# Kernel tuning notes

Hardware: AMD Instinct MI355X
Metric: run time of the kernel (lower is better)

The kernel has to match this reference:

```python
import jax, jax.numpy as jnp
import numpy as np

N, E = 100000, 800000
IN, HID, H, C, L, OUT = 32, 128, 4, 32, 3, 5
NEG_SLOPE = 0.2
EPS = 1e-5


def setup_inputs() -> dict:
    key = jax.random.key(0)
    ks = jax.random.split(key, 20)
    s = 0.1
    inp = {
        "x": jax.random.normal(ks[0], (N, IN), jnp.float32),
        "edge_index": jax.random.randint(ks[1], (2, E), 0, N, jnp.int64),
        "edge_attr": jax.random.uniform(ks[2], (E, 1), jnp.float32),
        "Win": jax.random.normal(ks[3], (IN, HID), jnp.float32) * s,
        "b_in": jnp.zeros((HID,), jnp.float32),
        "Wg": jax.random.normal(ks[4], (L, HID, H * C), jnp.float32) * s,
        "bg": jnp.zeros((L, H * C), jnp.float32),
        "a_src": jax.random.normal(ks[5], (L, H, C), jnp.float32) * s,
        "a_dst": jax.random.normal(ks[6], (L, H, C), jnp.float32) * s,
        "We": jax.random.normal(ks[7], (L, 1, H * C), jnp.float32) * s,
        "a_edge": jax.random.normal(ks[8], (L, H, C), jnp.float32) * s,
        "ln_w": jnp.ones((L, HID), jnp.float32),
        "ln_b": jnp.zeros((L, HID), jnp.float32),
        "Wout": jax.random.normal(ks[9], (HID, OUT), jnp.float32) * s,
        "bout": jnp.zeros((OUT,), jnp.float32),
    }
    return inp


def _add_self_loops(src, dst, ea):
    # PyG fill_value='mean': self-loop attr = mean of incoming edge attrs per node
    ones = jnp.ones((src.shape[0],), ea.dtype)
    deg = jax.ops.segment_sum(ones, dst, N)
    loop_attr = jax.ops.segment_sum(ea, dst, N) / jnp.maximum(deg, 1.0)[:, None]
    idx = jnp.arange(N, dtype=src.dtype)
    return (jnp.concatenate([src, idx]), jnp.concatenate([dst, idx]),
            jnp.concatenate([ea, loop_attr], axis=0))


def _gat_conv(x, src, dst, ea, Wg, bg, a_s, a_d, We, a_e):
    xh = (x @ Wg).reshape(N, H, C)                    # [N,H,C]
    al_s = jnp.einsum('nhc,hc->nh', xh, a_s)          # [N,H]
    al_d = jnp.einsum('nhc,hc->nh', xh, a_d)
    ee = (ea @ We).reshape(-1, H, C)                  # [Et,H,C]
    al_e = jnp.einsum('ehc,hc->eh', ee, a_e)
    logits = jax.nn.leaky_relu(al_s[src] + al_d[dst] + al_e, NEG_SLOPE)
    m = jax.ops.segment_max(logits, dst, N)
    m = jnp.where(jnp.isfinite(m), m, 0.0)
    ex = jnp.exp(logits - m[dst])
    den = jax.ops.segment_sum(ex, dst, N)
    alpha = ex / (den[dst] + 1e-16)                   # segment softmax over dst
    out = jax.ops.segment_sum(alpha[:, :, None] * xh[src], dst, N)
    return out.reshape(N, H * C) + bg


def _graph_layernorm(h, w, b):
    # PyG LayerNorm(mode='graph'): normalize over all nodes and features
    h = h - jnp.mean(h)
    var = jnp.mean(h * h)
    return h / jnp.sqrt(var + EPS) * w + b


def reference(x, edge_index, edge_attr, Win, b_in, Wg, bg, a_src, a_dst, We,
              a_edge, ln_w, ln_b, Wout, bout):
    src, dst = edge_index[0], edge_index[1]
    src, dst, ea = _add_self_loops(src, dst, edge_attr)
    h = x @ Win + b_in
    for l in range(L):
        g = _gat_conv(h, src, dst, ea, Wg[l], bg[l], a_src[l], a_dst[l],
                      We[l], a_edge[l])
        g = _graph_layernorm(g, ln_w[l], ln_b[l])
        h = jax.nn.relu(g + h)
    return h @ Wout + bout
```

## Files before the change

kernel.cpp:

```cpp
#include <hip/hip_runtime.h>
#include <hip/hip_bf16.h>

#define NN 100000
#define EE 800000
#define HID 128
#define NH 4
#define CH 32
#define NL 3
#define NOUT 5
#define NEG_SLOPE 0.2f
#define LN_EPS 1e-5f
#define GCAP 64
#define NB_SCAN 98
#define HQ (HID / 2)
#define WB_LSZ 9216
#define HB 3125
#define NG64 1563

typedef unsigned int u32;
typedef __attribute__((ext_vector_type(8))) short bf16x8;
typedef __attribute__((ext_vector_type(4))) float f32x4;

static __device__ __forceinline__ float bflo(u32 r) { return __uint_as_float(r << 16); }
static __device__ __forceinline__ float bfhi(u32 r) { return __uint_as_float(r & 0xffff0000u); }
static __device__ __forceinline__ unsigned short f2bf(float x) {
    union U { __hip_bfloat16 b; unsigned short s; } u;
    u.b = __float2bfloat16(x);
    return u.s;
}
static __device__ __forceinline__ u32 pack2(float a, float b) {
    return (u32)f2bf(a) | ((u32)f2bf(b) << 16);
}
static __device__ __forceinline__ float lrelu(float x) {
    return x > 0.f ? x : NEG_SLOPE * x;
}

__global__ void hist_prep_kernel(const int* __restrict__ ei, int* __restrict__ cnt,
                                 u32* __restrict__ slot,
                                 const float* __restrict__ We, const float* __restrict__ a_e,
                                 float* __restrict__ wedot,
                                 const float* __restrict__ Win, const float* __restrict__ b_in,
                                 const float* __restrict__ Wg, float* __restrict__ wf,
                                 const float* __restrict__ a_src, const float* __restrict__ a_dst,
                                 u32* __restrict__ wb, float* __restrict__ wga) {
    int b = blockIdx.x, t = threadIdx.x;
    if (b < HB) {
        int e = b * 256 + t;
        if (e >= EE) return;
        int d = ei[EE + e];
        int s = atomicAdd(&cnt[d], 1);
        slot[e] = ((u32)d << 8) | (u32)s;
        return;
    }
    if (b == HB) {
        if (t < NL * NH) {
            int l = t >> 2, hh = t & 3;
            float s = 0.f;
            #pragma unroll
            for (int c = 0; c < CH; c++)
                s += We[l * HID + hh * CH + c] * a_e[l * HID + hh * CH + c];
            wedot[t] = s;
        }
        for (int i = t; i < HID * 8; i += 256) {
            int m = i >> 3, j = i & 7;
            int hh = j & 3;
            const float* a = (j < 4) ? (a_src + hh * CH) : (a_dst + hh * CH);
            const float* wrow = Wg + (size_t)m * HID + hh * CH;
            float s = 0.f;
            #pragma unroll
            for (int c = 0; c < CH; c++) s += wrow[c] * a[c];
            wga[i] = s;
        }
        return;
    }
    if (b < HB + 18) {
        int idx = (b - HB - 1) * 256 + t;
        if (idx >= 33 * HID) return;
        int r = idx >> 7, c = idx & 127;
        float acc = 0.f;
        for (int k = 0; k < HID; k++) {
            float a = (r < 32) ? Win[r * HID + k] : b_in[k];
            acc += a * Wg[(size_t)k * HID + c];
        }
        wf[r * HID + c] = acc;
        return;
    }
    {
        int idx = (b - HB - 18) * 256 + t;
        if (idx >= 2 * 2304) return;
        int l = idx / 2304;
        int rem = idx % 2304;
        int ks = rem / 576;
        int ct = (rem % 576) / 64;
        int lane = rem % 64;
        int q = lane >> 4, n = lane & 15;
        const float* W = Wg + (size_t)(l + 1) * HID * HID;
        float v[8];
        if (ct < 8) {
            #pragma unroll
            for (int j = 0; j < 8; j++) {
                int k = ks * 32 + q * 8 + j;
                v[j] = W[(size_t)k * HID + ct * 16 + n];
            }
        } else {
            #pragma unroll
            for (int j = 0; j < 8; j++) v[j] = 0.f;
            if (n < 8) {
                const float* a = (n < 4) ? (a_src + (l + 1) * HID + (n & 3) * CH)
                                         : (a_dst + (l + 1) * HID + (n & 3) * CH);
                #pragma unroll
                for (int j = 0; j < 8; j++) {
                    int k = ks * 32 + q * 8 + j;
                    const float* wrow = W + (size_t)k * HID + (n & 3) * CH;
                    float s = 0.f;
                    for (int c = 0; c < CH; c++) s += wrow[c] * a[c];
                    v[j] = s;
                }
            }
        }
        u32* dst = wb + (size_t)l * WB_LSZ + (size_t)((ks * 9 + ct) * 64 + lane) * 4;
        dst[0] = pack2(v[0], v[1]); dst[1] = pack2(v[2], v[3]);
        dst[2] = pack2(v[4], v[5]); dst[3] = pack2(v[6], v[7]);
    }
}

__global__ __launch_bounds__(1024) void scan1_kernel(const int* __restrict__ cnt,
                                                     int* __restrict__ rowptr,
                                                     int* __restrict__ bsum) {
    __shared__ int ws[16];
    int gid = blockIdx.x * 1024 + threadIdx.x;
    int v = (gid < NN) ? cnt[gid] : 0;
    int lane = threadIdx.x & 63, wid = threadIdx.x >> 6;
    int s = v;
    #pragma unroll
    for (int off = 1; off < 64; off <<= 1) {
        int t = __shfl_up(s, off, 64);
        if (lane >= off) s += t;
    }
    if (lane == 63) ws[wid] = s;
    __syncthreads();
    int add = 0;
    for (int w2 = 0; w2 < wid; w2++) add += ws[w2];
    int incl = s + add;
    if (gid <= NN) rowptr[gid] = incl - v;
    if (threadIdx.x == 1023) bsum[blockIdx.x] = incl;
}

__global__ void scan2_prep2_kernel(int* __restrict__ bsum,
                                   const float* __restrict__ Win,
                                   const float* __restrict__ b_in,
                                   const float* __restrict__ wga,
                                   float* __restrict__ wf, u32* __restrict__ wb2) {
    if (blockIdx.x == 0) {
        __shared__ int w0tot_s;
        int tid = threadIdx.x;
        int v = (tid < NB_SCAN) ? bsum[tid] : 0;
        int lane = tid & 63, wid = tid >> 6;
        int s = v;
        #pragma unroll
        for (int off = 1; off < 64; off <<= 1) {
            int t = __shfl_up(s, off, 64);
            if (lane >= off) s += t;
        }
        if (wid == 0 && lane == 63) w0tot_s = s;
        __syncthreads();
        int incl = s + (wid ? w0tot_s : 0);
        if (tid < NB_SCAN) bsum[tid] = incl - v;
        return;
    }
    int b = blockIdx.x - 1;
    int lane = threadIdx.x;
    if (lane >= 64) return;
    int q = lane >> 4, n = lane & 15;
    if (b == 17) {
        if (lane < 8) {
            float s = 0.f;
            for (int m = 0; m < HID; m++) s += b_in[m] * wga[m * 8 + lane];
            wf[33 * HID + lane] = s;
        }
        return;
    }
    float v[8];
    if (b < 8) {
        #pragma unroll
        for (int j = 0; j < 8; j++) v[j] = Win[(q * 8 + j) * HID + b * 16 + n];
    } else if (b < 16) {
        int ct = b - 8;
        #pragma unroll
        for (int j = 0; j < 8; j++) v[j] = wf[(q * 8 + j) * HID + ct * 16 + n];
    } else {
        #pragma unroll
        for (int j = 0; j < 8; j++) v[j] = 0.f;
        if (n < 8) {
            #pragma unroll
            for (int j = 0; j < 8; j++) {
                const float* wrow = Win + (q * 8 + j) * HID;
                float s = 0.f;
                for (int m = 0; m < HID; m++) s += wrow[m] * wga[m * 8 + n];
                v[j] = s;
            }
        }
    }
    u32* dst = wb2 + (size_t)(b * 64 + lane) * 4;
    dst[0] = pack2(v[0], v[1]); dst[1] = pack2(v[2], v[3]);
    dst[2] = pack2(v[4], v[5]); dst[3] = pack2(v[6], v[7]);
}

__global__ void scan3_kernel(int* __restrict__ rowptr, const int* __restrict__ bsum) {
    int gid = blockIdx.x * 1024 + threadIdx.x;
    if (gid <= NN) rowptr[gid] += bsum[blockIdx.x];
}

__global__ __launch_bounds__(256) void scatter_ingemm_kernel(
        const int* __restrict__ ei, const float* __restrict__ ea,
        const int* __restrict__ rowptr, const u32* __restrict__ slot,
        uint2* __restrict__ edges,
        const float* __restrict__ x, const u32* __restrict__ wb2,
        const float* __restrict__ wf, const float* __restrict__ b_in,
        u32* __restrict__ h, u32* __restrict__ xh,
        float* __restrict__ al_s, float* __restrict__ al_d) {
    __shared__ u32 xsu[1024];
    if (blockIdx.x < HB) {
        int e = blockIdx.x * 256 + threadIdx.x;
        if (e >= EE) return;
        u32 p = slot[e];
        int d = (int)(p >> 8);
        int pos = rowptr[d] + (int)(p & 255u);
        edges[pos] = make_uint2((u32)ei[e], __float_as_uint(ea[e]));
        return;
    }
    int t = threadIdx.x;
    int wv = t >> 6, lane = t & 63;
    int q = lane >> 4, n16 = lane & 15;
    int n0 = (blockIdx.x - HB) * 64;
    {
        int row = t >> 2, qq = t & 3;
        int gr = n0 + row;
        int rt = row >> 4, m = row & 15;
        uint4 op = make_uint4(0u, 0u, 0u, 0u);
        if (gr < NN) {
            float4 vA = *(const float4*)&x[(size_t)gr * 32 + qq * 8];
            float4 vB = *(const float4*)&x[(size_t)gr * 32 + qq * 8 + 4];
            op.x = pack2(vA.x, vA.y); op.y = pack2(vA.z, vA.w);
            op.z = pack2(vB.x, vB.y); op.w = pack2(vB.z, vB.w);
        }
        *(uint4*)&xsu[(rt * 64 + qq * 16 + m) * 4] = op;
    }
    bf16x8 bwin[2], bwf[2], bal;
    #pragma unroll
    for (int cc = 0; cc < 2; cc++) {
        uint4 r0 = *(const uint4*)&wb2[(size_t)(((wv * 2 + cc)) * 64 + lane) * 4];
        uint4 r1 = *(const uint4*)&wb2[(size_t)((8 + wv * 2 + cc) * 64 + lane) * 4];
        bwin[cc] = __builtin_bit_cast(bf16x8, r0);
        bwf[cc]  = __builtin_bit_cast(bf16x8, r1);
    }
    {
        uint4 r = *(const uint4*)&wb2[(size_t)(16 * 64 + lane) * 4];
        bal = __builtin_bit_cast(bf16x8, r);
    }
    __syncthreads();
    f32x4 acch[4][2], accx[4][2], accal[4];
    #pragma unroll
    for (int rt = 0; rt < 4; rt++) {
        acch[rt][0] = (f32x4){0.f, 0.f, 0.f, 0.f};
        acch[rt][1] = (f32x4){0.f, 0.f, 0.f, 0.f};
        accx[rt][0] = (f32x4){0.f, 0.f, 0.f, 0.f};
        accx[rt][1] = (f32x4){0.f, 0.f, 0.f, 0.f};
        accal[rt]   = (f32x4){0.f, 0.f, 0.f, 0.f};
    }
    #pragma unroll
    for (int rt = 0; rt < 4; rt++) {
        uint4 araw = *(const uint4*)&xsu[(rt * 64 + lane) * 4];
        bf16x8 af = __builtin_bit_cast(bf16x8, araw);
        acch[rt][0] = __builtin_amdgcn_mfma_f32_16x16x32_bf16(af, bwin[0], acch[rt][0], 0, 0, 0);
        acch[rt][1] = __builtin_amdgcn_mfma_f32_16x16x32_bf16(af, bwin[1], acch[rt][1], 0, 0, 0);
        accx[rt][0] = __builtin_amdgcn_mfma_f32_16x16x32_bf16(af, bwf[0], accx[rt][0], 0, 0, 0);
        accx[rt][1] = __builtin_amdgcn_mfma_f32_16x16x32_bf16(af, bwf[1], accx[rt][1], 0, 0, 0);
        if (wv == 3)
            accal[rt] = __builtin_amdgcn_mfma_f32_16x16x32_bf16(af, bal, accal[rt], 0, 0, 0);
    }
    float bi[2], bfv[2];
    #pragma unroll
    for (int cc = 0; cc < 2; cc++) {
        int col = (wv * 2 + cc) * 16 + n16;
        bi[cc] = b_in[col];
        bfv[cc] = wf[32 * HID + col];
    }
    float bfa = (wv == 3 && n16 < 8) ? wf[33 * HID + n16] : 0.f;
    #pragma unroll
    for (int rt = 0; rt < 4; rt++) {
        #pragma unroll
        for (int reg = 0; reg < 4; reg++) {
            int row = n0 + rt * 16 + q * 4 + reg;
            #pragma unroll
            for (int cc = 0; cc < 2; cc++) {
                float v = acch[rt][cc][reg] + bi[cc];
                float vp = __shfl_xor(v, 1, 64);
                float u = accx[rt][cc][reg] + bfv[cc];
                float up = __shfl_xor(u, 1, 64);
                if (!(n16 & 1) && row < NN) {
                    int colp = (wv * 2 + cc) * 8 + (n16 >> 1);
                    h[(size_t)row * HQ + colp] = pack2(v, vp);
                    xh[(size_t)row * HQ + colp] = pack2(u, up);
                }
            }
            if (wv == 3 && row < NN && n16 < 8) {
                float v = accal[rt][reg] + bfa;
                if (n16 < 4) al_s[row * 4 + n16] = v;
                else         al_d[row * 4 + (n16 - 4)] = v;
            }
        }
    }
}

__global__ __launch_bounds__(256) void gemm_mfma_kernel(const u32* __restrict__ h,
        const u32* __restrict__ wb, u32* __restrict__ xh, const u32* __restrict__ g,
        const float* __restrict__ lnw, const float* __restrict__ lnb,
        const float* __restrict__ partials, u32* __restrict__ hout,
        float* __restrict__ al_s, float* __restrict__ al_d) {
    __shared__ u32 hsu[4096];
    __shared__ float sred[8];
    int n0 = blockIdx.x * 64;
    int t = threadIdx.x;
    int wv = t >> 6, lane = t & 63;
    int q = lane >> 4, n16 = lane & 15;

    {
        const float4* pp = (const float4*)partials;
        float4 v0 = pp[t * 2], v1 = pp[t * 2 + 1];
        float s = v0.x + v0.z + v1.x + v1.z;
        float qq = v0.y + v0.w + v1.y + v1.w;
        #pragma unroll
        for (int off = 1; off <= 32; off <<= 1) {
            s += __shfl_xor(s, off, 64);
            qq += __shfl_xor(qq, off, 64);
        }
        if (lane == 0) { sred[wv * 2] = s; sred[wv * 2 + 1] = qq; }
    }
    __syncthreads();
    float S = sred[0] + sred[2] + sred[4] + sred[6];
    float Q = sred[1] + sred[3] + sred[5] + sred[7];
    const float M = (float)NN * (float)HID;
    float mean = S / M;
    float rstd = rsqrtf(fmaxf(Q / M - mean * mean, 0.f) + LN_EPS);

    bf16x8 bfrag[2][4];
    #pragma unroll
    for (int ks = 0; ks < 4; ks++) {
        #pragma unroll
        for (int cc = 0; cc < 2; cc++) {
            int ct = wv * 2 + cc;
            uint4 r = *(const uint4*)&wb[(size_t)((ks * 9 + ct) * 64 + lane) * 4];
            bfrag[cc][ks] = __builtin_bit_cast(bf16x8, r);
        }
    }
    bf16x8 bal[4];
    #pragma unroll
    for (int ks = 0; ks < 4; ks++) {
        uint4 r = *(const uint4*)&wb[(size_t)((ks * 9 + 8) * 64 + lane) * 4];
        bal[ks] = __builtin_bit_cast(bf16x8, r);
    }

    {
        int row = t >> 2;
        int qq = t & 3;
        int gr = n0 + row;
        int rt = row >> 4, m = row & 15;
        #pragma unroll
        for (int ks = 0; ks < 4; ks++) {
            int kk = ks * 32 + qq * 8;
            uint4 op = make_uint4(0u, 0u, 0u, 0u);
            if (gr < NN) {
                size_t base = (size_t)gr * HQ + (kk >> 1);
                uint4 gp = *(const uint4*)&g[base];
                uint4 hp = *(const uint4*)&h[base];
                float4 wA = *(const float4*)&lnw[kk];
                float4 wB = *(const float4*)&lnw[kk + 4];
                float4 bA = *(const float4*)&lnb[kk];
                float4 bB = *(const float4*)&lnb[kk + 4];
                float v0 = fmaxf((bflo(gp.x) - mean) * rstd * wA.x + bA.x + bflo(hp.x), 0.f);
                float v1 = fmaxf((bfhi(gp.x) - mean) * rstd * wA.y + bA.y + bfhi(hp.x), 0.f);
                float v2 = fmaxf((bflo(gp.y) - mean) * rstd * wA.z + bA.z + bflo(hp.y), 0.f);
                float v3 = fmaxf((bfhi(gp.y) - mean) * rstd * wA.w + bA.w + bfhi(hp.y), 0.f);
                float v4 = fmaxf((bflo(gp.z) - mean) * rstd * wB.x + bB.x + bflo(hp.z), 0.f);
                float v5 = fmaxf((bfhi(gp.z) - mean) * rstd * wB.y + bB.y + bfhi(hp.z), 0.f);
                float v6 = fmaxf((bflo(gp.w) - mean) * rstd * wB.z + bB.z + bflo(hp.w), 0.f);
                float v7 = fmaxf((bfhi(gp.w) - mean) * rstd * wB.w + bB.w + bfhi(hp.w), 0.f);
                op.x = pack2(v0, v1); op.y = pack2(v2, v3);
                op.z = pack2(v4, v5); op.w = pack2(v6, v7);
                *(uint4*)&hout[base] = op;
            }
            *(uint4*)&hsu[((rt * 4 + ks) * 64 + qq * 16 + m) * 4] = op;
        }
    }
    __syncthreads();

    f32x4 acc[4][2];
    f32x4 accal[4];
    #pragma unroll
    for (int rt = 0; rt < 4; rt++) {
        acc[rt][0] = (f32x4){0.f, 0.f, 0.f, 0.f};
        acc[rt][1] = (f32x4){0.f, 0.f, 0.f, 0.f};
        accal[rt]  = (f32x4){0.f, 0.f, 0.f, 0.f};
    }
    #pragma unroll
    for (int rt = 0; rt < 4; rt++) {
        #pragma unroll
        for (int ks = 0; ks < 4; ks++) {
            uint4 araw = *(const uint4*)&hsu[((rt * 4 + ks) * 64 + lane) * 4];
            bf16x8 af = __builtin_bit_cast(bf16x8, araw);
            acc[rt][0] = __builtin_amdgcn_mfma_f32_16x16x32_bf16(af, bfrag[0][ks], acc[rt][0], 0, 0, 0);
            acc[rt][1] = __builtin_amdgcn_mfma_f32_16x16x32_bf16(af, bfrag[1][ks], acc[rt][1], 0, 0, 0);
            if (wv == 3)
                accal[rt] = __builtin_amdgcn_mfma_f32_16x16x32_bf16(af, bal[ks], accal[rt], 0, 0, 0);
        }
    }

    #pragma unroll
    for (int rt = 0; rt < 4; rt++) {
        #pragma unroll
        for (int reg = 0; reg < 4; reg++) {
            int row = n0 + rt * 16 + q * 4 + reg;
            #pragma unroll
            for (int cc = 0; cc < 2; cc++) {
                float v = acc[rt][cc][reg];
                float vp = __shfl_xor(v, 1, 64);
                if (!(n16 & 1) && row < NN) {
                    int colp = (wv * 2 + cc) * 8 + (n16 >> 1);
                    xh[(size_t)row * HQ + colp] = pack2(v, vp);
                }
            }
            if (wv == 3 && row < NN && n16 < 8) {
                float v = accal[rt][reg];
                if (n16 < 4) al_s[row * 4 + n16] = v;
                else         al_d[row * 4 + (n16 - 4)] = v;
            }
        }
    }
}

__global__ __launch_bounds__(256) void gat_agg_kernel(const int* __restrict__ rowptr,
        const uint2* __restrict__ edges, const u32* __restrict__ xh,
        const float* __restrict__ al_s, const float* __restrict__ al_d,
        const float* __restrict__ wedot, const float* __restrict__ bg,
        u32* __restrict__ g, float* __restrict__ partials) {
    __shared__ float lds_ex[4][GCAP * 4];
    __shared__ float lds_ea[4][GCAP];
    __shared__ int lds_src[4][GCAP];
    int wv = threadIdx.x >> 6, lane = threadIdx.x & 63;
    int base = (blockIdx.x * 4 + wv) * 4;
    if (base >= NN) return;
    float* ex_w = lds_ex[wv];
    float* ea_w = lds_ea[wv];
    int* src_w = lds_src[wv];
    int b1 = base + 1 < NN ? base + 1 : NN;
    int b2 = base + 2 < NN ? base + 2 : NN;
    int b3 = base + 3 < NN ? base + 3 : NN;
    int b4 = base + 4 < NN ? base + 4 : NN;
    int r0 = rowptr[base], r1 = rowptr[b1], r2 = rowptr[b2], r3 = rowptr[b3], r4 = rowptr[b4];
    int span = r4 - r0;
    int ncached = span < GCAP ? span : GCAP;
    float wd0 = wedot[0], wd1 = wedot[1], wd2 = wedot[2], wd3 = wedot[3];

    for (int i = lane; i < ncached; i += 64) {
        int gi = r0 + i;
        uint2 e = edges[gi];
        int s = (int)e.x;
        float eav = __uint_as_float(e.y);
        int d = (gi >= r1) + (gi >= r2) + (gi >= r3);
        float4 aldv = *(const float4*)&al_d[(base + d) * 4];
        float4 als = *(const float4*)&al_s[s * 4];
        float e0 = __expf(lrelu(als.x + aldv.x + eav * wd0));
        float e1 = __expf(lrelu(als.y + aldv.y + eav * wd1));
        float e2 = __expf(lrelu(als.z + aldv.z + eav * wd2));
        float e3 = __expf(lrelu(als.w + aldv.w + eav * wd3));
        src_w[i] = s;
        ea_w[i] = eav;
        *(float4*)&ex_w[i * 4] = make_float4(e0, e1, e2, e3);
    }

    int nl = lane >> 4, cg = lane & 15;
    int n = base + nl;
    bool nvalid = n < NN;
    int ls = (nl == 0 ? r0 : nl == 1 ? r1 : nl == 2 ? r2 : r3) - r0;
    int le = (nl == 0 ? r1 : nl == 1 ? r2 : nl == 2 ? r3 : r4) - r0;
    int lec = le < ncached ? le : ncached;
    int head = cg >> 2;
    int c4 = cg * 4;
    float wdh = head == 0 ? wd0 : head == 1 ? wd1 : head == 2 ? wd2 : wd3;
    float a0 = 0.f, a1 = 0.f, a2 = 0.f, a3 = 0.f;
    float a4 = 0.f, a5 = 0.f, a6 = 0.f, a7 = 0.f, den = 0.f, easum = 0.f;
    int j = ls;
    for (; j + 3 < lec; j += 4) {
        int s0 = src_w[j], s1 = src_w[j + 1], s2 = src_w[j + 2], s3 = src_w[j + 3];
        float e0 = ex_w[j * 4 + head],       e1 = ex_w[(j + 1) * 4 + head];
        float e2 = ex_w[(j + 2) * 4 + head], e3 = ex_w[(j + 3) * 4 + head];
        uint4 x0 = *(const uint4*)&xh[(size_t)s0 * HQ + c4];
        uint4 x1 = *(const uint4*)&xh[(size_t)s1 * HQ + c4];
        uint4 x2 = *(const uint4*)&xh[(size_t)s2 * HQ + c4];
        uint4 x3 = *(const uint4*)&xh[(size_t)s3 * HQ + c4];
        den += e0 + e1 + e2 + e3;
        easum += ea_w[j] + ea_w[j + 1] + ea_w[j + 2] + ea_w[j + 3];
        a0 += e0 * bflo(x0.x); a1 += e0 * bfhi(x0.x);
        a2 += e0 * bflo(x0.y); a3 += e0 * bfhi(x0.y);
        a4 += e0 * bflo(x0.z); a5 += e0 * bfhi(x0.z);
        a6 += e0 * bflo(x0.w); a7 += e0 * bfhi(x0.w);
        a0 += e1 * bflo(x1.x); a1 += e1 * bfhi(x1.x);
        a2 += e1 * bflo(x1.y); a3 += e1 * bfhi(x1.y);
        a4 += e1 * bflo(x1.z); a5 += e1 * bfhi(x1.z);
        a6 += e1 * bflo(x1.w); a7 += e1 * bfhi(x1.w);
        a0 += e2 * bflo(x2.x); a1 += e2 * bfhi(x2.x);
        a2 += e2 * bflo(x2.y); a3 += e2 * bfhi(x2.y);
        a4 += e2 * bflo(x2.z); a5 += e2 * bfhi(x2.z);
        a6 += e2 * bflo(x2.w); a7 += e2 * bfhi(x2.w);
        a0 += e3 * bflo(x3.x); a1 += e3 * bfhi(x3.x);
        a2 += e3 * bflo(x3.y); a3 += e3 * bfhi(x3.y);
        a4 += e3 * bflo(x3.z); a5 += e3 * bfhi(x3.z);
        a6 += e3 * bflo(x3.w); a7 += e3 * bfhi(x3.w);
    }
    for (; j < lec; j++) {
        int s0 = src_w[j];
        float e0 = ex_w[j * 4 + head];
        uint4 x0 = *(const uint4*)&xh[(size_t)s0 * HQ + c4];
        den += e0;
        easum += ea_w[j];
        a0 += e0 * bflo(x0.x); a1 += e0 * bfhi(x0.x);
        a2 += e0 * bflo(x0.y); a3 += e0 * bfhi(x0.y);
        a4 += e0 * bflo(x0.z); a5 += e0 * bfhi(x0.z);
        a6 += e0 * bflo(x0.w); a7 += e0 * bfhi(x0.w);
    }
    if (le > lec && nvalid) {
        float aldh = al_d[n * 4 + head];
        for (int jt = (ls > lec ? ls : lec); jt < le; jt++) {
            uint2 e = edges[r0 + jt];
            int s = (int)e.x;
            float eav = __uint_as_float(e.y);
            float ex = __expf(lrelu(al_s[s * 4 + head] + aldh + eav * wdh));
            den += ex;
            easum += eav;
            uint4 x0 = *(const uint4*)&xh[(size_t)s * HQ + c4];
            a0 += ex * bflo(x0.x); a1 += ex * bfhi(x0.x);
            a2 += ex * bflo(x0.y); a3 += ex * bfhi(x0.y);
            a4 += ex * bflo(x0.z); a5 += ex * bfhi(x0.z);
            a6 += ex * bflo(x0.w); a7 += ex * bfhi(x0.w);
        }
    }
    if (nvalid) {
        float mea = easum / fmaxf((float)(le - ls), 1.0f);
        float alh = al_s[n * 4 + head] + al_d[n * 4 + head];
        float ex = __expf(lrelu(alh + mea * wdh));
        den += ex;
        uint4 x0 = *(const uint4*)&xh[(size_t)n * HQ + c4];
        a0 += ex * bflo(x0.x); a1 += ex * bfhi(x0.x);
        a2 += ex * bflo(x0.y); a3 += ex * bfhi(x0.y);
        a4 += ex * bflo(x0.z); a5 += ex * bfhi(x0.z);
        a6 += ex * bflo(x0.w); a7 += ex * bfhi(x0.w);
    }

    float inv = 1.0f / (den + 1e-16f);
    int c0 = cg * 8;
    float4 bgA = *(const float4*)&bg[c0];
    float4 bgB = *(const float4*)&bg[c0 + 4];
    float o0 = a0 * inv + bgA.x, o1 = a1 * inv + bgA.y;
    float o2 = a2 * inv + bgA.z, o3 = a3 * inv + bgA.w;
    float o4 = a4 * inv + bgB.x, o5 = a5 * inv + bgB.y;
    float o6 = a6 * inv + bgB.z, o7 = a7 * inv + bgB.w;
    float ss = 0.f, sq = 0.f;
    if (nvalid) {
        uint4 op;
        op.x = pack2(o0, o1); op.y = pack2(o2, o3);
        op.z = pack2(o4, o5); op.w = pack2(o6, o7);
        *(uint4*)&g[(size_t)n * HQ + c4] = op;
        ss = o0 + o1 + o2 + o3 + o4 + o5 + o6 + o7;
        sq = o0 * o0 + o1 * o1 + o2 * o2 + o3 * o3
           + o4 * o4 + o5 * o5 + o6 * o6 + o7 * o7;
    }
    #pragma unroll
    for (int off = 1; off <= 32; off <<= 1) {
        ss += __shfl_xor(ss, off, 64);
        sq += __shfl_xor(sq, off, 64);
    }
    if (lane == 0) {
        int sl = ((blockIdx.x * 4 + wv) & 1023) * 2;
        atomicAdd(&partials[sl], ss);
        atomicAdd(&partials[sl + 1], sq);
    }
}

__global__ __launch_bounds__(256) void ln_out_kernel(const u32* __restrict__ g,
        const u32* __restrict__ h, const float* __restrict__ lnw,
        const float* __restrict__ lnb, const float* __restrict__ partials,
        const float* __restrict__ Wout, const float* __restrict__ bout,
        float* __restrict__ out) {
    __shared__ float wsh[HID * NOUT];
    __shared__ float sred[8];
    int t = threadIdx.x;
    int wv = t >> 6, lane = t & 63;
    {
        const float4* pp = (const float4*)partials;
        float4 v0 = pp[t * 2], v1 = pp[t * 2 + 1];
        float s = v0.x + v0.z + v1.x + v1.z;
        float qq = v0.y + v0.w + v1.y + v1.w;
        #pragma unroll
        for (int off = 1; off <= 32; off <<= 1) {
            s += __shfl_xor(s, off, 64);
            qq += __shfl_xor(qq, off, 64);
        }
        if (lane == 0) { sred[wv * 2] = s; sred[wv * 2 + 1] = qq; }
    }
    for (int i = t; i < HID * NOUT; i += 256) wsh[i] = Wout[i];
    __syncthreads();
    float S = sred[0] + sred[2] + sred[4] + sred[6];
    float Q = sred[1] + sred[3] + sred[5] + sred[7];
    const float M = (float)NN * (float)HID;
    float mean = S / M;
    float rstd = rsqrtf(fmaxf(Q / M - mean * mean, 0.f) + LN_EPS);

    int nl = lane >> 4, cg = lane & 15;
    int n = (blockIdx.x * 4 + wv) * 4 + nl;
    bool nvalid = n < NN;
    float p[NOUT] = {};
    if (nvalid) {
        int c0 = cg * 8;
        uint4 gv = *(const uint4*)&g[(size_t)n * HQ + cg * 4];
        uint4 hv = *(const uint4*)&h[(size_t)n * HQ + cg * 4];
        float4 wA = *(const float4*)&lnw[c0], wB = *(const float4*)&lnw[c0 + 4];
        float4 bA = *(const float4*)&lnb[c0], bB = *(const float4*)&lnb[c0 + 4];
        float o[8];
        o[0] = fmaxf((bflo(gv.x) - mean) * rstd * wA.x + bA.x + bflo(hv.x), 0.f);
        o[1] = fmaxf((bfhi(gv.x) - mean) * rstd * wA.y + bA.y + bfhi(hv.x), 0.f);
        o[2] = fmaxf((bflo(gv.y) - mean) * rstd * wA.z + bA.z + bflo(hv.y), 0.f);
        o[3] = fmaxf((bfhi(gv.y) - mean) * rstd * wA.w + bA.w + bfhi(hv.y), 0.f);
        o[4] = fmaxf((bflo(gv.z) - mean) * rstd * wB.x + bB.x + bflo(hv.z), 0.f);
        o[5] = fmaxf((bfhi(gv.z) - mean) * rstd * wB.y + bB.y + bfhi(hv.z), 0.f);
        o[6] = fmaxf((bflo(gv.w) - mean) * rstd * wB.z + bB.z + bflo(hv.w), 0.f);
        o[7] = fmaxf((bfhi(gv.w) - mean) * rstd * wB.w + bB.w + bfhi(hv.w), 0.f);
        #pragma unroll
        for (int jj = 0; jj < NOUT; jj++) {
            float acc = 0.f;
            #pragma unroll
            for (int k = 0; k < 8; k++) acc += o[k] * wsh[(c0 + k) * NOUT + jj];
            p[jj] = acc;
        }
    }
    #pragma unroll
    for (int off = 1; off <= 8; off <<= 1) {
        #pragma unroll
        for (int jj = 0; jj < NOUT; jj++) p[jj] += __shfl_xor(p[jj], off, 64);
    }
    if (cg == 0 && nvalid) {
        #pragma unroll
        for (int jj = 0; jj < NOUT; jj++)
            out[(size_t)n * NOUT + jj] = p[jj] + bout[jj];
    }
}

extern "C" void kernel_launch(void* const* d_in, const int* in_sizes, int n_in,
                              void* d_out, int out_size, void* d_ws, size_t ws_size,
                              hipStream_t stream) {
    const float* x      = (const float*)d_in[0];
    const int*   ei     = (const int*)d_in[1];
    const float* ea     = (const float*)d_in[2];
    const float* Win    = (const float*)d_in[3];
    const float* b_in   = (const float*)d_in[4];
    const float* Wg     = (const float*)d_in[5];
    const float* bg     = (const float*)d_in[6];
    const float* a_src  = (const float*)d_in[7];
    const float* a_dst  = (const float*)d_in[8];
    const float* We     = (const float*)d_in[9];
    const float* a_edge = (const float*)d_in[10];
    const float* ln_w   = (const float*)d_in[11];
    const float* ln_b   = (const float*)d_in[12];
    const float* Wout   = (const float*)d_in[13];
    const float* bout   = (const float*)d_in[14];
    float* out = (float*)d_out;

    char* w = (char*)d_ws;
    size_t off = 0;
    auto alloc = [&](size_t bytes) -> void* {
        void* p = w + off;
        off = (off + bytes + 255) & ~(size_t)255;
        return p;
    };
    int*   cnt     = (int*)alloc(NN * sizeof(int));
    float* partials = (float*)alloc(3 * 2048 * sizeof(float));
    size_t zero_span = off;
    u32*   slot    = (u32*)alloc((size_t)EE * sizeof(u32));
    int*   rowptr  = (int*)alloc((NN + 1) * sizeof(int));
    int*   bsum    = (int*)alloc(NB_SCAN * sizeof(int));
    uint2* edges   = (uint2*)alloc((size_t)EE * sizeof(uint2));
    u32*   h       = (u32*)alloc((size_t)NN * HQ * sizeof(u32));
    u32*   g       = (u32*)alloc((size_t)NN * HQ * sizeof(u32));
    u32*   xh      = (u32*)alloc((size_t)NN * HQ * sizeof(u32));
    float* al_s    = (float*)alloc((size_t)NN * NH * sizeof(float));
    float* al_d    = (float*)alloc((size_t)NN * NH * sizeof(float));
    float* wedot   = (float*)alloc(16 * sizeof(float));
    float* wf      = (float*)alloc(34 * HID * sizeof(float));
    float* wga     = (float*)alloc(HID * 8 * sizeof(float));
    u32*   wb      = (u32*)alloc((size_t)2 * WB_LSZ * sizeof(u32));
    u32*   wb2     = (u32*)alloc(17 * 64 * 4 * sizeof(u32));
    (void)ws_size; (void)n_in; (void)in_sizes; (void)out_size;

    hipMemsetAsync(d_ws, 0, zero_span, stream);
    hist_prep_kernel<<<HB + 36, 256, 0, stream>>>(ei, cnt, slot, We, a_edge, wedot,
                                                  Win, b_in, Wg, wf, a_src, a_dst,
                                                  wb, wga);
    scan1_kernel<<<NB_SCAN, 1024, 0, stream>>>(cnt, rowptr, bsum);
    scan2_prep2_kernel<<<19, 128, 0, stream>>>(bsum, Win, b_in, wga, wf, wb2);
    scan3_kernel<<<NB_SCAN, 1024, 0, stream>>>(rowptr, bsum);
    scatter_ingemm_kernel<<<HB + NG64, 256, 0, stream>>>(ei, ea, rowptr, slot, edges,
                                                         x, wb2, wf, b_in, h, xh,
                                                         al_s, al_d);
    for (int l = 0; l < NL; l++) {
        if (l > 0) {
            gemm_mfma_kernel<<<NG64, 256, 0, stream>>>(
                h, wb + (size_t)(l - 1) * WB_LSZ, xh, g,
                ln_w + (size_t)(l - 1) * HID, ln_b + (size_t)(l - 1) * HID,
                partials + (size_t)(l - 1) * 2048, h, al_s, al_d);
        }
        gat_agg_kernel<<<(NN + 15) / 16, 256, 0, stream>>>(
            rowptr, edges, xh, al_s, al_d, wedot + l * 4,
            bg + (size_t)l * HID, g, partials + (size_t)l * 2048);
    }

    ln_out_kernel<<<(NN + 15) / 16, 256, 0, stream>>>(g, h, ln_w + (size_t)2 * HID,
                                                      ln_b + (size_t)2 * HID,
                                                      partials + 2 * 2048, Wout, bout, out);
}
```

Baseline: 394.5 us.

## Replace three-pass scan with single-pass decoupled look-back and coarsen edge blocks

The separate scan1/scan2/scan3 kernels are merged into one kernel that computes the rowptr prefix sum with a decoupled look-back across blocks, using flag/sum/prefix arrays zeroed by the existing memset. The weight-prep work that lived in scan2 moves into extra blocks of the same launch. The histogram and scatter phases now process four edges per thread with a quarter of the blocks. This removes two kernel launches and their dependencies, at the cost of spin-waiting on earlier blocks, which depends on those blocks being scheduled first.

```diff
diff --git a/kernel.cpp b/kernel.cpp
--- a/kernel.cpp
+++ b/kernel.cpp
@@ -14,7 +14,8 @@
 #define NB_SCAN 98
 #define HQ (HID / 2)
 #define WB_LSZ 9216
-#define HB 3125
+#define HB4 782
+#define SB4 782
 #define NG64 1563
 
 typedef unsigned int u32;
@@ -44,15 +45,20 @@
                                  const float* __restrict__ a_src, const float* __restrict__ a_dst,
                                  u32* __restrict__ wb, float* __restrict__ wga) {
     int b = blockIdx.x, t = threadIdx.x;
-    if (b < HB) {
-        int e = b * 256 + t;
-        if (e >= EE) return;
-        int d = ei[EE + e];
-        int s = atomicAdd(&cnt[d], 1);
-        slot[e] = ((u32)d << 8) | (u32)s;
+    if (b < HB4) {
+        int e0 = b * 1024 + t;
+        #pragma unroll
+        for (int k = 0; k < 4; k++) {
+            int e = e0 + k * 256;
+            if (e < EE) {
+                int d = ei[EE + e];
+                int s = atomicAdd(&cnt[d], 1);
+                slot[e] = ((u32)d << 8) | (u32)s;
+            }
+        }
         return;
     }
-    if (b == HB) {
+    if (b == HB4) {
         if (t < NL * NH) {
             int l = t >> 2, hh = t & 3;
             float s = 0.f;
@@ -73,8 +79,8 @@
         }
         return;
     }
-    if (b < HB + 18) {
-        int idx = (b - HB - 1) * 256 + t;
+    if (b < HB4 + 18) {
+        int idx = (b - HB4 - 1) * 256 + t;
         if (idx >= 33 * HID) return;
         int r = idx >> 7, c = idx & 127;
         float acc = 0.f;
@@ -86,7 +92,7 @@
         return;
     }
     {
-        int idx = (b - HB - 18) * 256 + t;
+        int idx = (b - HB4 - 18) * 256 + t;
         if (idx >= 2 * 2304) return;
         int l = idx / 2304;
         int rem = idx % 2304;
@@ -124,91 +130,88 @@
     }
 }
 
-__global__ __launch_bounds__(1024) void scan1_kernel(const int* __restrict__ cnt,
-                                                     int* __restrict__ rowptr,
-                                                     int* __restrict__ bsum) {
+__global__ __launch_bounds__(1024) void scan_prep2_kernel(const int* __restrict__ cnt,
+        int* __restrict__ rowptr, int* __restrict__ sums, int* __restrict__ prefixes,
+        int* __restrict__ flags,
+        const float* __restrict__ Win, const float* __restrict__ b_in,
+        const float* __restrict__ wga, float* __restrict__ wf, u32* __restrict__ wb2) {
+    if (blockIdx.x >= NB_SCAN) {
+        int b = blockIdx.x - NB_SCAN;
+        int lane = threadIdx.x;
+        if (lane >= 64) return;
+        int q = lane >> 4, n = lane & 15;
+        if (b == 17) {
+            if (lane < 8) {
+                float s = 0.f;
+                for (int m = 0; m < HID; m++) s += b_in[m] * wga[m * 8 + lane];
+                wf[33 * HID + lane] = s;
+            }
+            return;
+        }
+        float v[8];
+        if (b < 8) {
+            #pragma unroll
+            for (int j = 0; j < 8; j++) v[j] = Win[(q * 8 + j) * HID + b * 16 + n];
+        } else if (b < 16) {
+            int ct = b - 8;
+            #pragma unroll
+            for (int j = 0; j < 8; j++) v[j] = wf[(q * 8 + j) * HID + ct * 16 + n];
+        } else {
+            #pragma unroll
+            for (int j = 0; j < 8; j++) v[j] = 0.f;
+            if (n < 8) {
+                #pragma unroll
+                for (int j = 0; j < 8; j++) {
+                    const float* wrow = Win + (q * 8 + j) * HID;
+                    float s = 0.f;
+                    for (int m = 0; m < HID; m++) s += wrow[m] * wga[m * 8 + n];
+                    v[j] = s;
+                }
+            }
+        }
+        u32* dst = wb2 + (size_t)(b * 64 + lane) * 4;
+        dst[0] = pack2(v[0], v[1]); dst[1] = pack2(v[2], v[3]);
+        dst[2] = pack2(v[4], v[5]); dst[3] = pack2(v[6], v[7]);
+        return;
+    }
     __shared__ int ws[16];
-    int gid = blockIdx.x * 1024 + threadIdx.x;
+    __shared__ int bprefix;
+    int b = blockIdx.x;
+    int gid = b * 1024 + threadIdx.x;
     int v = (gid < NN) ? cnt[gid] : 0;
     int lane = threadIdx.x & 63, wid = threadIdx.x >> 6;
     int s = v;
     #pragma unroll
     for (int off = 1; off < 64; off <<= 1) {
-        int t = __shfl_up(s, off, 64);
-        if (lane >= off) s += t;
+        int t2 = __shfl_up(s, off, 64);
+        if (lane >= off) s += t2;
     }
     if (lane == 63) ws[wid] = s;
     __syncthreads();
     int add = 0;
     for (int w2 = 0; w2 < wid; w2++) add += ws[w2];
     int incl = s + add;
-    if (gid <= NN) rowptr[gid] = incl - v;
-    if (threadIdx.x == 1023) bsum[blockIdx.x] = incl;
-}
-
-__global__ void scan2_prep2_kernel(int* __restrict__ bsum,
-                                   const float* __restrict__ Win,
-                                   const float* __restrict__ b_in,
-                                   const float* __restrict__ wga,
-                                   float* __restrict__ wf, u32* __restrict__ wb2) {
-    if (blockIdx.x == 0) {
-        __shared__ int w0tot_s;
-        int tid = threadIdx.x;
-        int v = (tid < NB_SCAN) ? bsum[tid] : 0;
-        int lane = tid & 63, wid = tid >> 6;
-        int s = v;
-        #pragma unroll
-        for (int off = 1; off < 64; off <<= 1) {
-            int t = __shfl_up(s, off, 64);
-            if (lane >= off) s += t;
-        }
-        if (wid == 0 && lane == 63) w0tot_s = s;
-        __syncthreads();
-        int incl = s + (wid ? w0tot_s : 0);
-        if (tid < NB_SCAN) bsum[tid] = incl - v;
-        return;
-    }
-    int b = blockIdx.x - 1;
-    int lane = threadIdx.x;
-    if (lane >= 64) return;
-    int q = lane >> 4, n = lane & 15;
-    if (b == 17) {
-        if (lane < 8) {
-            float s = 0.f;
-            for (int m = 0; m < HID; m++) s += b_in[m] * wga[m * 8 + lane];
-            wf[33 * HID + lane] = s;
-        }
-        return;
-    }
-    float v[8];
-    if (b < 8) {
-        #pragma unroll
-        for (int j = 0; j < 8; j++) v[j] = Win[(q * 8 + j) * HID + b * 16 + n];
-    } else if (b < 16) {
-        int ct = b - 8;
-        #pragma unroll
-        for (int j = 0; j < 8; j++) v[j] = wf[(q * 8 + j) * HID + ct * 16 + n];
-    } else {
-        #pragma unroll
-        for (int j = 0; j < 8; j++) v[j] = 0.f;
-        if (n < 8) {
-            #pragma unroll
-            for (int j = 0; j < 8; j++) {
-                const float* wrow = Win + (q * 8 + j) * HID;
-                float s = 0.f;
-                for (int m = 0; m < HID; m++) s += wrow[m] * wga[m * 8 + n];
-                v[j] = s;
-            }
-        }
-    }
-    u32* dst = wb2 + (size_t)(b * 64 + lane) * 4;
-    dst[0] = pack2(v[0], v[1]); dst[1] = pack2(v[2], v[3]);
-    dst[2] = pack2(v[4], v[5]); dst[3] = pack2(v[6], v[7]);
-}
-
-__global__ void scan3_kernel(int* __restrict__ rowptr, const int* __restrict__ bsum) {
-    int gid = blockIdx.x * 1024 + threadIdx.x;
-    if (gid <= NN) rowptr[gid] += bsum[blockIdx.x];
+    if (threadIdx.x == 0) {
+        int total = 0;
+        for (int w2 = 0; w2 < 16; w2++) total += ws[w2];
+        atomicExch(&sums[b], total);
+        __threadfence();
+        atomicExch(&flags[b], 1);
+        int pfx = 0;
+        for (int i = b - 1; i >= 0; i--) {
+            int f;
+            do { f = atomicAdd(&flags[i], 0); } while (f == 0);
+            if (f == 2) { pfx += atomicAdd(&prefixes[i], 0); break; }
+            pfx += atomicAdd(&sums[i], 0);
+        }
+        atomicExch(&prefixes[b], pfx + total);
+        __threadfence();
+        atomicExch(&flags[b], 2);
+        bprefix = pfx;
+    }
+    __syncthreads();
+    int pfx = bprefix;
+    if (gid <= NN) rowptr[gid] = pfx + incl - v;
 }
 
 __global__ __launch_bounds__(256) void scatter_ingemm_kernel(
@@ -220,19 +223,24 @@
         u32* __restrict__ h, u32* __restrict__ xh,
         float* __restrict__ al_s, float* __restrict__ al_d) {
     __shared__ u32 xsu[1024];
-    if (blockIdx.x < HB) {
-        int e = blockIdx.x * 256 + threadIdx.x;
-        if (e >= EE) return;
-        u32 p = slot[e];
-        int d = (int)(p >> 8);
-        int pos = rowptr[d] + (int)(p & 255u);
-        edges[pos] = make_uint2((u32)ei[e], __float_as_uint(ea[e]));
+    if (blockIdx.x < SB4) {
+        int e0 = blockIdx.x * 1024 + threadIdx.x;
+        #pragma unroll
+        for (int k = 0; k < 4; k++) {
+            int e = e0 + k * 256;
+            if (e < EE) {
+                u32 p = slot[e];
+                int d = (int)(p >> 8);
+                int pos = rowptr[d] + (int)(p & 255u);
+                edges[pos] = make_uint2((u32)ei[e], __float_as_uint(ea[e]));
+            }
+        }
         return;
     }
     int t = threadIdx.x;
     int wv = t >> 6, lane = t & 63;
     int q = lane >> 4, n16 = lane & 15;
-    int n0 = (blockIdx.x - HB) * 64;
+    int n0 = (blockIdx.x - SB4) * 64;
     {
         int row = t >> 2, qq = t & 3;
         int gr = n0 + row;
@@ -682,12 +690,14 @@
         off = (off + bytes + 255) & ~(size_t)255;
         return p;
     };
-    int*   cnt     = (int*)alloc(NN * sizeof(int));
+    int*   cnt      = (int*)alloc(NN * sizeof(int));
     float* partials = (float*)alloc(3 * 2048 * sizeof(float));
+    int*   sums     = (int*)alloc(NB_SCAN * sizeof(int));
+    int*   prefixes = (int*)alloc(NB_SCAN * sizeof(int));
+    int*   flags    = (int*)alloc(NB_SCAN * sizeof(int));
     size_t zero_span = off;
     u32*   slot    = (u32*)alloc((size_t)EE * sizeof(u32));
     int*   rowptr  = (int*)alloc((NN + 1) * sizeof(int));
-    int*   bsum    = (int*)alloc(NB_SCAN * sizeof(int));
     uint2* edges   = (uint2*)alloc((size_t)EE * sizeof(uint2));
     u32*   h       = (u32*)alloc((size_t)NN * HQ * sizeof(u32));
     u32*   g       = (u32*)alloc((size_t)NN * HQ * sizeof(u32));
@@ -702,15 +712,14 @@
     (void)ws_size; (void)n_in; (void)in_sizes; (void)out_size;
 
     hipMemsetAsync(d_ws, 0, zero_span, stream);
-    hist_prep_kernel<<<HB + 36, 256, 0, stream>>>(ei, cnt, slot, We, a_edge, wedot,
-                                                  Win, b_in, Wg, wf, a_src, a_dst,
-                                                  wb, wga);
-    scan1_kernel<<<NB_SCAN, 1024, 0, stream>>>(cnt, rowptr, bsum);
-    scan2_prep2_kernel<<<19, 128, 0, stream>>>(bsum, Win, b_in, wga, wf, wb2);
-    scan3_kernel<<<NB_SCAN, 1024, 0, stream>>>(rowptr, bsum);
-    scatter_ingemm_kernel<<<HB + NG64, 256, 0, stream>>>(ei, ea, rowptr, slot, edges,
-                                                         x, wb2, wf, b_in, h, xh,
-                                                         al_s, al_d);
+    hist_prep_kernel<<<HB4 + 36, 256, 0, stream>>>(ei, cnt, slot, We, a_edge, wedot,
+                                                   Win, b_in, Wg, wf, a_src, a_dst,
+                                                   wb, wga);
+    scan_prep2_kernel<<<NB_SCAN + 18, 1024, 0, stream>>>(cnt, rowptr, sums, prefixes,
+                                                         flags, Win, b_in, wga, wf, wb2);
+    scatter_ingemm_kernel<<<SB4 + NG64, 256, 0, stream>>>(ei, ea, rowptr, slot, edges,
+                                                          x, wb2, wf, b_in, h, xh,
+                                                          al_s, al_d);
     for (int l = 0; l < NL; l++) {
         if (l > 0) {
             gemm_mfma_kernel<<<NG64, 256, 0, stream>>>(
```

Result: no change. 390.0 us (-1.1%).
